# Performance work log

Measured on AMD Instinct MI355X. Metric: run time of the kernel, lower is better.

## Reference

```python
import jax, jax.numpy as jnp
import numpy as np

MASK_VALUE = -10000000.0


def setup_inputs() -> dict:
    key = jax.random.key(0)
    ks = jax.random.split(key, 8)
    U, I, J, C, E = 128, 256, 512, 128, 128
    return {
        "target_items_context": jax.random.normal(ks[0], (U, I, C), jnp.float32),
        "interacted_items_context": jax.random.normal(ks[1], (U, J, C), jnp.float32),
        "user_embeds": jax.random.normal(ks[2], (U, E), jnp.float32),
        "attention_mask": jax.random.randint(ks[3], (U, J), 0, 2) > 0,
        "w_dense": jax.random.normal(ks[4], (2 * C,), jnp.float32) * 0.02,
        "b_dense": jax.random.normal(ks[5], (1,), jnp.float32) * 0.02,
        "W_mlp": jax.random.normal(ks[6], (E + C, C), jnp.float32) * 0.02,
        "b_mlp": jax.random.normal(ks[7], (C,), jnp.float32) * 0.02,
    }


def reference(target_items_context, interacted_items_context, user_embeds,
              attention_mask, w_dense, b_dense, W_mlp, b_mlp):
    C = target_items_context.shape[-1]
    E = user_embeds.shape[-1]
    # additive attention score: tanh([t; k] @ w + b) = tanh(t@w1 + k@w2 + b)
    # (dropout is identity in eval mode)
    s_t = jnp.einsum('uic,c->ui', target_items_context, w_dense[:C])      # (U, I)
    s_k = jnp.einsum('ujc,c->uj', interacted_items_context, w_dense[C:])  # (U, J)
    scores = jnp.tanh(s_t[:, :, None] + s_k[:, None, :] + b_dense[0])     # (U, I, J)
    scores = scores + (~attention_mask)[:, None, :].astype(scores.dtype) * MASK_VALUE
    attn = jax.nn.softmax(scores, axis=-1)                                # (U, I, J)
    # weighted pooling of interacted contexts
    pooled = jnp.einsum('uij,ujc->uic', attn, interacted_items_context)   # (U, I, C)
    # mlp: relu([user; pooled] @ W + b) = relu(user@W[:E] + pooled@W[E:] + b)
    u_part = user_embeds @ W_mlp[:E]                                      # (U, C)
    user_context = jax.nn.relu(u_part[:, None, :] + pooled @ W_mlp[E:] + b_mlp)
    return user_context, attn
```

## Files before the change

kernel.cpp:

```cpp
#include <hip/hip_runtime.h>

#define UU 128
#define II 256
#define JJ 512
#define CC 128
#define EE 128
#define IB 16
#define NIB 16
#define JT 64
#define NJT 8
#define VTP 72

typedef short bf16x8 __attribute__((ext_vector_type(8)));
typedef float f32x4 __attribute__((ext_vector_type(4)));

union FragU { bf16x8 v; unsigned u[4]; };

__device__ __forceinline__ float fast_tanh(float x) {
    float ex = __expf(2.0f * x);
    return 1.0f - 2.0f / (ex + 1.0f);
}

__device__ __forceinline__ unsigned pack_bf16x2(float lo, float hi) {
    unsigned ul = __float_as_uint(lo), uh = __float_as_uint(hi);
    ul = (ul + 0x7FFFu + ((ul >> 16) & 1u)) >> 16;
    uh = (uh + 0x7FFFu + ((uh >> 16) & 1u)) >> 16;
    return ul | (uh << 16);
}

__device__ __forceinline__ short bf16s(float f) {
    unsigned u = __float_as_uint(f);
    u = (u + 0x7FFFu + ((u >> 16) & 1u)) >> 16;
    return (short)u;
}

__device__ __forceinline__ float wave_reduce_add(float v) {
#pragma unroll
    for (int k = 32; k >= 1; k >>= 1) v += __shfl_xor(v, k, 64);
    return v;
}

#define VT_BLOCKS (UU * NJT)
#define UP_BLOCKS (UU * CC / 256)

__global__ void precompute_kernel(const float* __restrict__ itc,
                                  const float* __restrict__ user,
                                  const float* __restrict__ wd,
                                  const float* __restrict__ Wm,
                                  const float* __restrict__ bm,
                                  float* __restrict__ sk_g,
                                  float* __restrict__ up_g,
                                  short* __restrict__ vtg,
                                  short* __restrict__ wtg) {
    __shared__ float vt_f[JT][CC + 4];
    int b = blockIdx.x;
    int t = threadIdx.x;
    if (b < VT_BLOCKS) {
        int u = b & 127, jt = b >> 7;
        const float* src = itc + ((size_t)u * JJ + jt * JT) * CC;
#pragma unroll
        for (int k = 0; k < 8; ++k) {
            int f = t + 256 * k;
            int row = f >> 5, c4 = (f & 31) * 4;
            f32x4 v = __builtin_nontemporal_load(
                (const f32x4*)&src[(size_t)row * CC + c4]);
            *(f32x4*)&vt_f[row][c4] = v;
        }
        __syncthreads();
        {
            int r = t >> 2, q4 = t & 3;
            float s = 0.f;
#pragma unroll
            for (int cc = 0; cc < 32; cc += 4) {
                float4 a = *(const float4*)&vt_f[r][q4 * 32 + cc];
                float4 w = *(const float4*)&wd[CC + q4 * 32 + cc];
                s += a.x * w.x + a.y * w.y + a.z * w.z + a.w * w.w;
            }
            s += __shfl_xor(s, 1, 64);
            s += __shfl_xor(s, 2, 64);
            if (q4 == 0) sk_g[u * JJ + jt * JT + r] = s;
        }
        {
            int c = t & 127, half = t >> 7;
            unsigned* dst = (unsigned*)(vtg + (size_t)(u * NJT + jt) * 8192) +
                            half * 2048 + c * 16;
#pragma unroll
            for (int m4 = 0; m4 < 4; ++m4) {
                unsigned q[4];
#pragma unroll
                for (int mm = 0; mm < 4; ++mm) {
                    int m = 4 * m4 + mm;
                    q[mm] = pack_bf16x2(vt_f[32 * half + 2 * m][c],
                                        vt_f[32 * half + 2 * m + 1][c]);
                }
                *(uint4*)&dst[4 * m4] = make_uint4(q[0], q[1], q[2], q[3]);
            }
        }
    } else if (b < VT_BLOCKS + UP_BLOCKS) {
        int idx = (b - VT_BLOCKS) * 256 + t;
        int u = idx >> 7, c = idx & 127;
        float acc = bm[c];
#pragma unroll 8
        for (int e = 0; e < EE; ++e) acc += user[u * EE + e] * Wm[e * CC + c];
        up_g[idx] = acc;
    } else {
        int n = t & 127, khalf = t >> 7;
#pragma unroll
        for (int ks2 = 0; ks2 < 2; ++ks2) {
            int ks = khalf * 2 + ks2;
#pragma unroll
            for (int g = 0; g < 4; ++g) {
                unsigned q[4];
#pragma unroll
                for (int pr = 0; pr < 4; ++pr) {
                    float lo = Wm[(size_t)(EE + 32 * ks + 8 * g + 2 * pr) * CC + n];
                    float hi = Wm[(size_t)(EE + 32 * ks + 8 * g + 2 * pr + 1) * CC + n];
                    q[pr] = pack_bf16x2(lo, hi);
                }
                *(uint4*)&wtg[ks * 4096 + n * 32 + 8 * g] =
                    make_uint4(q[0], q[1], q[2], q[3]);
            }
        }
    }
}

__global__ __launch_bounds__(256, 6) void fused_main(
    const float* __restrict__ tgt, const int* __restrict__ mask,
    const float* __restrict__ wd, const float* __restrict__ bd,
    const float* __restrict__ sk_g, const float* __restrict__ up_g,
    const short* __restrict__ vt_g, const short* __restrict__ wt_g,
    float* __restrict__ out_ctx, float* __restrict__ out_attn) {
    __shared__ __align__(16) short ps[8192];
    __shared__ __align__(16) short pooled_bf[2048];
    __shared__ float dinv_lds[IB];

    int b = blockIdx.x;
    int x = b & 7, qq = b >> 3;
    int u = x + 8 * (qq >> 4);
    int ib = qq & 15;
    int i0 = ib * IB;
    int t = threadIdx.x;
    int w = t >> 6, l = t & 63, ln = l & 15, g = l >> 4;
    int r = t >> 4, s4 = t & 15;

    float sv;
    {
        const float* trow = tgt + ((size_t)(u * II + i0 + r)) * CC + s4 * 8;
        f32x4 t0 = __builtin_nontemporal_load((const f32x4*)&trow[0]);
        f32x4 t1 = __builtin_nontemporal_load((const f32x4*)&trow[4]);
        float4 w0 = *(const float4*)&wd[s4 * 8];
        float4 w1 = *(const float4*)&wd[s4 * 8 + 4];
        float part = t0[0] * w0.x + t0[1] * w0.y + t0[2] * w0.z + t0[3] * w0.w +
                     t1[0] * w1.x + t1[1] * w1.y + t1[2] * w1.z + t1[3] * w1.w;
        part += __shfl_xor(part, 1, 64);
        part += __shfl_xor(part, 2, 64);
        part += __shfl_xor(part, 4, 64);
        part += __shfl_xor(part, 8, 64);
        sv = part + bd[0];
    }

    const float* skb = sk_g + u * JJ;
    const int* mkb = mask + u * JJ;
    float rowsum = 0.f;
#pragma unroll
    for (int h = 0; h < 4; ++h) {
        int jb = 8 * (s4 + 16 * h);
        float4 k0 = *(const float4*)&skb[jb];
        float4 k1 = *(const float4*)&skb[jb + 4];
        int4 m0 = *(const int4*)&mkb[jb];
        int4 m1 = *(const int4*)&mkb[jb + 4];
        float p0 = m0.x ? __expf(fast_tanh(sv + k0.x)) : 0.f;
        float p1 = m0.y ? __expf(fast_tanh(sv + k0.y)) : 0.f;
        float p2 = m0.z ? __expf(fast_tanh(sv + k0.z)) : 0.f;
        float p3 = m0.w ? __expf(fast_tanh(sv + k0.w)) : 0.f;
        float p4 = m1.x ? __expf(fast_tanh(sv + k1.x)) : 0.f;
        float p5 = m1.y ? __expf(fast_tanh(sv + k1.y)) : 0.f;
        float p6 = m1.z ? __expf(fast_tanh(sv + k1.z)) : 0.f;
        float p7 = m1.w ? __expf(fast_tanh(sv + k1.w)) : 0.f;
        rowsum += p0 + p1 + p2 + p3 + p4 + p5 + p6 + p7;
        unsigned q0 = pack_bf16x2(p0, p1);
        unsigned q1 = pack_bf16x2(p2, p3);
        unsigned q2 = pack_bf16x2(p4, p5);
        unsigned q3 = pack_bf16x2(p6, p7);
        int gp = (s4 + 16 * h) ^ (r & 7);
        *(uint4*)((char*)ps + r * 1024 + 16 * gp) = make_uint4(q0, q1, q2, q3);
    }
    rowsum += __shfl_xor(rowsum, 1, 64);
    rowsum += __shfl_xor(rowsum, 2, 64);
    rowsum += __shfl_xor(rowsum, 4, 64);
    rowsum += __shfl_xor(rowsum, 8, 64);
    float dinv = 1.0f / rowsum;
    if (s4 == 0) dinv_lds[r] = dinv;

    const short* b_base =
        vt_g + (size_t)u * (NJT * 8192) + (32 * w + ln) * 32 + 8 * g;
    bf16x8 pb0[4], pb1[4];
#pragma unroll
    for (int s = 0; s < 4; ++s) {
        int off = (s >> 1) * 8192 + (s & 1) * 4096;
        pb0[s] = *(const bf16x8*)&b_base[off];
        pb1[s] = *(const bf16x8*)&b_base[off + 512];
    }

    {
        float* ab = out_attn + ((size_t)(u * II + i0 + r)) * JJ;
#pragma unroll
        for (int h = 0; h < 4; ++h) {
            int gp = (s4 + 16 * h) ^ (r & 7);
            uint4 q = *(const uint4*)((char*)ps + r * 1024 + 16 * gp);
            int jb = 8 * (s4 + 16 * h);
            f32x4 v0, v1;
            v0[0] = __uint_as_float(q.x << 16) * dinv;
            v0[1] = __uint_as_float(q.x & 0xFFFF0000u) * dinv;
            v0[2] = __uint_as_float(q.y << 16) * dinv;
            v0[3] = __uint_as_float(q.y & 0xFFFF0000u) * dinv;
            v1[0] = __uint_as_float(q.z << 16) * dinv;
            v1[1] = __uint_as_float(q.z & 0xFFFF0000u) * dinv;
            v1[2] = __uint_as_float(q.w << 16) * dinv;
            v1[3] = __uint_as_float(q.w & 0xFFFF0000u) * dinv;
            __builtin_nontemporal_store(v0, (f32x4*)&ab[jb]);
            __builtin_nontemporal_store(v1, (f32x4*)&ab[jb + 4]);
        }
    }

    asm volatile("s_waitcnt lgkmcnt(0)" ::: "memory");
    __builtin_amdgcn_s_barrier();
    asm volatile("" ::: "memory");

    f32x4 acc0 = {0.f, 0.f, 0.f, 0.f};
    f32x4 acc1 = {0.f, 0.f, 0.f, 0.f};
    __builtin_amdgcn_s_setprio(1);
#pragma unroll
    for (int s = 0; s < 16; ++s) {
        bf16x8 af = *(const bf16x8*)((const char*)ps + ln * 1024 +
                                     16 * ((4 * s + g) ^ (ln & 7)));
        acc0 = __builtin_amdgcn_mfma_f32_16x16x32_bf16(af, pb0[s & 3], acc0, 0, 0, 0);
        acc1 = __builtin_amdgcn_mfma_f32_16x16x32_bf16(af, pb1[s & 3], acc1, 0, 0, 0);
        if (s < 12) {
            int off = ((s + 4) >> 1) * 8192 + ((s + 4) & 1) * 4096;
            pb0[s & 3] = *(const bf16x8*)&b_base[off];
            pb1[s & 3] = *(const bf16x8*)&b_base[off + 512];
        }
    }
    __builtin_amdgcn_s_setprio(0);

    const short* wbase = wt_g + (32 * w + ln) * 32 + 8 * g;
    bf16x8 wb0[4], wb1[4];
#pragma unroll
    for (int ks = 0; ks < 4; ++ks) {
        wb0[ks] = *(const bf16x8*)&wbase[ks * 4096];
        wb1[ks] = *(const bf16x8*)&wbase[ks * 4096 + 512];
    }

#pragma unroll
    for (int ri = 0; ri < 4; ++ri) {
        int row = 4 * g + ri;
        float dv = dinv_lds[row];
        int c0 = 32 * w + ln;
        int by0 = row * 256 + 16 * ((c0 >> 3) ^ (row & 7)) + 2 * (ln & 7);
        *(short*)((char*)pooled_bf + by0) = bf16s(acc0[ri] * dv);
        int c1 = c0 + 16;
        int by1 = row * 256 + 16 * ((c1 >> 3) ^ (row & 7)) + 2 * (ln & 7);
        *(short*)((char*)pooled_bf + by1) = bf16s(acc1[ri] * dv);
    }
    asm volatile("s_waitcnt lgkmcnt(0)" ::: "memory");
    __builtin_amdgcn_s_barrier();
    asm volatile("" ::: "memory");

    f32x4 oa0 = {0.f, 0.f, 0.f, 0.f};
    f32x4 oa1 = {0.f, 0.f, 0.f, 0.f};
#pragma unroll
    for (int ks = 0; ks < 4; ++ks) {
        bf16x8 pa = *(const bf16x8*)((const char*)pooled_bf + ln * 256 +
                                     16 * ((4 * ks + g) ^ (ln & 7)));
        oa0 = __builtin_amdgcn_mfma_f32_16x16x32_bf16(pa, wb0[ks], oa0, 0, 0, 0);
        oa1 = __builtin_amdgcn_mfma_f32_16x16x32_bf16(pa, wb1[ks], oa1, 0, 0, 0);
    }
    {
        int c0 = 32 * w + ln, c1 = c0 + 16;
        float up0v = up_g[u * CC + c0];
        float up1v = up_g[u * CC + c1];
        float* ctx = out_ctx + ((size_t)(u * II + i0)) * CC;
#pragma unroll
        for (int ri = 0; ri < 4; ++ri) {
            int row = 4 * g + ri;
            __builtin_nontemporal_store(fmaxf(oa0[ri] + up0v, 0.f),
                                        &ctx[(size_t)row * CC + c0]);
            __builtin_nontemporal_store(fmaxf(oa1[ri] + up1v, 0.f),
                                        &ctx[(size_t)row * CC + c1]);
        }
    }
}

__global__ __launch_bounds__(256, 3) void fused_fallback(
    const float* __restrict__ tgt, const float* __restrict__ itc,
    const float* __restrict__ user, const int* __restrict__ mask,
    const float* __restrict__ wd, const float* __restrict__ bd,
    const float* __restrict__ Wm, const float* __restrict__ bm,
    float* __restrict__ out_ctx, float* __restrict__ out_attn) {
    __shared__ __align__(16) short Vt[CC][VTP];
    __shared__ __align__(16) float pool[IB][CC + 4];
    __shared__ __align__(16) float skv[JJ];
    __shared__ __align__(16) float stv[IB];
    __shared__ __align__(16) float upv[CC];
    __shared__ __align__(16) float dinv_lds[IB];
    __shared__ unsigned char mk[JJ];

    int b = blockIdx.x;
    int x = b & 7, q = b >> 3;
    int u = x + 8 * (q >> 4);
    int ib = q & 15;
    int i0 = ib * IB;
    int t = threadIdx.x;

    mk[t] = (unsigned char)(mask[u * JJ + t] != 0);
    mk[t + 256] = (unsigned char)(mask[u * JJ + t + 256] != 0);

    {
        int lane = t & 63, w4 = t >> 6;
        float2 w2 = *(const float2*)&wd[CC + lane * 2];
        for (int r = w4; r < JJ; r += 4) {
            float2 a = *(const float2*)&itc[((size_t)u * JJ + r) * CC + lane * 2];
            float s = wave_reduce_add(a.x * w2.x + a.y * w2.y);
            if (lane == 0) skv[r] = s;
        }
        float2 w1 = *(const float2*)&wd[lane * 2];
        float bdv = bd[0];
        for (int r = w4; r < IB; r += 4) {
            float2 a = *(const float2*)&tgt[((size_t)u * II + i0 + r) * CC + lane * 2];
            float s = wave_reduce_add(a.x * w1.x + a.y * w1.y);
            if (lane == 0) stv[r] = s + bdv;
        }
        if (t < CC) {
            float acc = bm[t];
            for (int e = 0; e < EE; ++e) acc += user[u * EE + e] * Wm[e * CC + t];
            upv[t] = acc;
        }
    }
    __syncthreads();

    const int l = t & 63;
    const int w = t >> 6;
    const int ln = l & 15;
    const int g = l >> 4;

    bf16x8 a[16];
    float rowsum = 0.0f;
    {
        float s = stv[ln];
#pragma unroll
        for (int t16 = 0; t16 < 16; ++t16) {
            int j = 32 * t16 + 8 * g;
            float4 k0 = *(const float4*)&skv[j];
            float4 k1 = *(const float4*)&skv[j + 4];
            unsigned m0 = *(const unsigned*)&mk[j];
            unsigned m1 = *(const unsigned*)&mk[j + 4];
            float pf[8];
            pf[0] = (m0 & 0x000000FFu) ? __expf(fast_tanh(s + k0.x)) : 0.0f;
            pf[1] = (m0 & 0x0000FF00u) ? __expf(fast_tanh(s + k0.y)) : 0.0f;
            pf[2] = (m0 & 0x00FF0000u) ? __expf(fast_tanh(s + k0.z)) : 0.0f;
            pf[3] = (m0 & 0xFF000000u) ? __expf(fast_tanh(s + k0.w)) : 0.0f;
            pf[4] = (m1 & 0x000000FFu) ? __expf(fast_tanh(s + k1.x)) : 0.0f;
            pf[5] = (m1 & 0x0000FF00u) ? __expf(fast_tanh(s + k1.y)) : 0.0f;
            pf[6] = (m1 & 0x00FF0000u) ? __expf(fast_tanh(s + k1.z)) : 0.0f;
            pf[7] = (m1 & 0xFF000000u) ? __expf(fast_tanh(s + k1.w)) : 0.0f;
            rowsum += pf[0] + pf[1] + pf[2] + pf[3] + pf[4] + pf[5] + pf[6] + pf[7];
            FragU cu;
            cu.u[0] = pack_bf16x2(pf[0], pf[1]);
            cu.u[1] = pack_bf16x2(pf[2], pf[3]);
            cu.u[2] = pack_bf16x2(pf[4], pf[5]);
            cu.u[3] = pack_bf16x2(pf[6], pf[7]);
            a[t16] = cu.v;
        }
    }
    rowsum += __shfl_xor(rowsum, 16, 64);
    rowsum += __shfl_xor(rowsum, 32, 64);
    float dinv = 1.0f / rowsum;
    if (t < 16) dinv_lds[t] = dinv;

    {
        float* abase = out_attn + ((size_t)(u * II + i0 + ln)) * JJ + 8 * g;
#pragma unroll
        for (int t16 = 0; t16 < 16; ++t16) {
            FragU cu; cu.v = a[t16];
            float f0 = __uint_as_float(cu.u[0] << 16) * dinv;
            float f1 = __uint_as_float(cu.u[0] & 0xFFFF0000u) * dinv;
            float f2 = __uint_as_float(cu.u[1] << 16) * dinv;
            float f3 = __uint_as_float(cu.u[1] & 0xFFFF0000u) * dinv;
            float f4 = __uint_as_float(cu.u[2] << 16) * dinv;
            float f5 = __uint_as_float(cu.u[2] & 0xFFFF0000u) * dinv;
            float f6 = __uint_as_float(cu.u[3] << 16) * dinv;
            float f7 = __uint_as_float(cu.u[3] & 0xFFFF0000u) * dinv;
            *(float4*)&abase[32 * t16] = make_float4(f0, f1, f2, f3);
            *(float4*)&abase[32 * t16 + 4] = make_float4(f4, f5, f6, f7);
        }
    }

    f32x4 acc0 = {0.f, 0.f, 0.f, 0.f};
    f32x4 acc1 = {0.f, 0.f, 0.f, 0.f};
    const float* Vu = itc + (size_t)u * JJ * CC;
    const int cg = t & 31;
    const int jp = t >> 5;
    const int n0 = w * 32;

    for (int jt = 0; jt < 8; ++jt) {
        int j0 = jt * JT;
        __syncthreads();
#pragma unroll
        for (int it = 0; it < 4; ++it) {
            int jl = 2 * (jp + 8 * it);
            const float* r0 = &Vu[(size_t)(j0 + jl) * CC];
            const float* r1 = r0 + CC;
#pragma unroll
            for (int qv = 0; qv < 4; ++qv) {
                int c = cg + 32 * qv;
                *(unsigned*)&Vt[c][jl] = pack_bf16x2(r0[c], r1[c]);
            }
        }
        __syncthreads();
#pragma unroll
        for (int kk = 0; kk < 2; ++kk) {
            bf16x8 b0 = *(const bf16x8*)&Vt[n0 + ln][32 * kk + 8 * g];
            bf16x8 b1 = *(const bf16x8*)&Vt[n0 + 16 + ln][32 * kk + 8 * g];
            acc0 = __builtin_amdgcn_mfma_f32_16x16x32_bf16(a[2 * jt + kk], b0,
                                                           acc0, 0, 0, 0);
            acc1 = __builtin_amdgcn_mfma_f32_16x16x32_bf16(a[2 * jt + kk], b1,
                                                           acc1, 0, 0, 0);
        }
    }

    __syncthreads();
    {
        float4 dv = *(const float4*)&dinv_lds[4 * g];
        float dvr[4] = {dv.x, dv.y, dv.z, dv.w};
#pragma unroll
        for (int r = 0; r < 4; ++r) {
            pool[4 * g + r][n0 + ln] = acc0[r] * dvr[r];
            pool[4 * g + r][n0 + 16 + ln] = acc1[r] * dvr[r];
        }
    }
    __syncthreads();

    {
        int tx = t & 15, ty = t >> 4;
        float o[8];
#pragma unroll
        for (int k = 0; k < 8; ++k) o[k] = 0.f;
#pragma unroll 4
        for (int k = 0; k < CC; ++k) {
            float pk = pool[ty][k];
            float4 w0 = *(const float4*)&Wm[(size_t)(EE + k) * CC + tx * 8];
            float4 w1 = *(const float4*)&Wm[(size_t)(EE + k) * CC + tx * 8 + 4];
            o[0] += pk * w0.x; o[1] += pk * w0.y; o[2] += pk * w0.z; o[3] += pk * w0.w;
            o[4] += pk * w1.x; o[5] += pk * w1.y; o[6] += pk * w1.z; o[7] += pk * w1.w;
        }
        float4 up0 = *(const float4*)&upv[tx * 8];
        float4 up1 = *(const float4*)&upv[tx * 8 + 4];
        float4 r0, r1;
        r0.x = fmaxf(o[0] + up0.x, 0.f); r0.y = fmaxf(o[1] + up0.y, 0.f);
        r0.z = fmaxf(o[2] + up0.z, 0.f); r0.w = fmaxf(o[3] + up0.w, 0.f);
        r1.x = fmaxf(o[4] + up1.x, 0.f); r1.y = fmaxf(o[5] + up1.y, 0.f);
        r1.z = fmaxf(o[6] + up1.z, 0.f); r1.w = fmaxf(o[7] + up1.w, 0.f);
        float* ctx = out_ctx + ((size_t)(u * II + i0 + ty)) * CC + tx * 8;
        *(float4*)&ctx[0] = r0;
        *(float4*)&ctx[4] = r1;
    }
}

extern "C" void kernel_launch(void* const* d_in, const int* in_sizes, int n_in,
                              void* d_out, int out_size, void* d_ws,
                              size_t ws_size, hipStream_t stream) {
    const float* tgt  = (const float*)d_in[0];
    const float* itc  = (const float*)d_in[1];
    const float* user = (const float*)d_in[2];
    const int*   mask = (const int*)d_in[3];
    const float* wd   = (const float*)d_in[4];
    const float* bd   = (const float*)d_in[5];
    const float* Wm   = (const float*)d_in[6];
    const float* bm   = (const float*)d_in[7];
    float* out_ctx  = (float*)d_out;
    float* out_attn = out_ctx + (size_t)UU * II * CC;

    size_t scalars = (size_t)(UU * JJ + UU * CC) * sizeof(float);
    size_t vt_bytes = (size_t)UU * NJT * 8192 * sizeof(short);
    size_t wt_bytes = (size_t)16384 * sizeof(short);
    size_t need = scalars + vt_bytes + wt_bytes;
    if (ws_size >= need) {
        float* sk_g = (float*)d_ws;
        float* up_g = sk_g + UU * JJ;
        short* vt_g = (short*)((char*)d_ws + scalars);
        short* wt_g = vt_g + (size_t)UU * NJT * 8192;
        int gridA = VT_BLOCKS + UP_BLOCKS + 1;
        precompute_kernel<<<gridA, 256, 0, stream>>>(itc, user, wd, Wm, bm,
                                                     sk_g, up_g, vt_g, wt_g);
        fused_main<<<UU * NIB, 256, 0, stream>>>(tgt, mask, wd, bd, sk_g, up_g,
                                                 vt_g, wt_g, out_ctx, out_attn);
    } else {
        fused_fallback<<<UU * NIB, 256, 0, stream>>>(
            tgt, itc, user, mask, wd, bd, Wm, bm, out_ctx, out_attn);
    }
}
```

Measured before the change: 58.06 us.

## Process 32 target rows per block to reuse V fragments across two MFMA tiles

The main fused kernel now handles 32 target rows per block instead of 16, halving the grid and reusing each loaded V (interacted-context) B-fragment and MLP weight fragment for two 16-row MFMA tiles. The attention-probability write-out moves after the pooling MFMA loop, now reads from LDS per row with a flat thread mapping, and the pooled buffer aliases the probability LDS region through an extra barrier. This cuts global loads of V and W per output row in exchange for doubled LDS use (32KB), fewer resident blocks per CU, and more registers per thread.

```diff
diff --git a/kernel.cpp b/kernel.cpp
--- a/kernel.cpp
+++ b/kernel.cpp
@@ -5,11 +5,12 @@
 #define JJ 512
 #define CC 128
 #define EE 128
-#define IB 16
-#define NIB 16
+#define IB2 32
+#define NIB2 8
 #define JT 64
 #define NJT 8
 #define VTP 72
+#define IBF 16
 
 typedef short bf16x8 __attribute__((ext_vector_type(8)));
 typedef float f32x4 __attribute__((ext_vector_type(4)));
@@ -124,47 +125,54 @@
     }
 }
 
-__global__ __launch_bounds__(256, 6) void fused_main(
+__global__ __launch_bounds__(256, 4) void fused_main(
     const float* __restrict__ tgt, const int* __restrict__ mask,
     const float* __restrict__ wd, const float* __restrict__ bd,
     const float* __restrict__ sk_g, const float* __restrict__ up_g,
     const short* __restrict__ vt_g, const short* __restrict__ wt_g,
     float* __restrict__ out_ctx, float* __restrict__ out_attn) {
-    __shared__ __align__(16) short ps[8192];
-    __shared__ __align__(16) short pooled_bf[2048];
-    __shared__ float dinv_lds[IB];
+    __shared__ __align__(16) short ps[16384];
+    __shared__ float dinv_lds[IB2];
 
     int b = blockIdx.x;
-    int x = b & 7, qq = b >> 3;
-    int u = x + 8 * (qq >> 4);
-    int ib = qq & 15;
-    int i0 = ib * IB;
+    int x = b & 7, q = b >> 3;
+    int u = x + 8 * (q >> 3);
+    int ib = q & 7;
+    int i0 = ib * IB2;
     int t = threadIdx.x;
     int w = t >> 6, l = t & 63, ln = l & 15, g = l >> 4;
-    int r = t >> 4, s4 = t & 15;
+    int r2 = t >> 3, seg8 = t & 7;
+    int tile = r2 >> 4, rr = r2 & 15;
 
     float sv;
     {
-        const float* trow = tgt + ((size_t)(u * II + i0 + r)) * CC + s4 * 8;
+        const float* trow = tgt + ((size_t)(u * II + i0 + r2)) * CC + seg8 * 16;
         f32x4 t0 = __builtin_nontemporal_load((const f32x4*)&trow[0]);
         f32x4 t1 = __builtin_nontemporal_load((const f32x4*)&trow[4]);
-        float4 w0 = *(const float4*)&wd[s4 * 8];
-        float4 w1 = *(const float4*)&wd[s4 * 8 + 4];
+        f32x4 t2 = __builtin_nontemporal_load((const f32x4*)&trow[8]);
+        f32x4 t3 = __builtin_nontemporal_load((const f32x4*)&trow[12]);
+        float4 w0 = *(const float4*)&wd[seg8 * 16];
+        float4 w1 = *(const float4*)&wd[seg8 * 16 + 4];
+        float4 w2 = *(const float4*)&wd[seg8 * 16 + 8];
+        float4 w3 = *(const float4*)&wd[seg8 * 16 + 12];
         float part = t0[0] * w0.x + t0[1] * w0.y + t0[2] * w0.z + t0[3] * w0.w +
-                     t1[0] * w1.x + t1[1] * w1.y + t1[2] * w1.z + t1[3] * w1.w;
+                     t1[0] * w1.x + t1[1] * w1.y + t1[2] * w1.z + t1[3] * w1.w +
+                     t2[0] * w2.x + t2[1] * w2.y + t2[2] * w2.z + t2[3] * w2.w +
+                     t3[0] * w3.x + t3[1] * w3.y + t3[2] * w3.z + t3[3] * w3.w;
         part += __shfl_xor(part, 1, 64);
         part += __shfl_xor(part, 2, 64);
         part += __shfl_xor(part, 4, 64);
-        part += __shfl_xor(part, 8, 64);
         sv = part + bd[0];
     }
 
     const float* skb = sk_g + u * JJ;
     const int* mkb = mask + u * JJ;
+    char* psrow = (char*)ps + tile * 16384 + rr * 1024;
     float rowsum = 0.f;
-#pragma unroll
-    for (int h = 0; h < 4; ++h) {
-        int jb = 8 * (s4 + 16 * h);
+#pragma unroll 4
+    for (int h = 0; h < 8; ++h) {
+        int gcol = seg8 + 8 * h;
+        int jb = gcol * 8;
         float4 k0 = *(const float4*)&skb[jb];
         float4 k1 = *(const float4*)&skb[jb + 4];
         int4 m0 = *(const int4*)&mkb[jb];
@@ -182,15 +190,13 @@
         unsigned q1 = pack_bf16x2(p2, p3);
         unsigned q2 = pack_bf16x2(p4, p5);
         unsigned q3 = pack_bf16x2(p6, p7);
-        int gp = (s4 + 16 * h) ^ (r & 7);
-        *(uint4*)((char*)ps + r * 1024 + 16 * gp) = make_uint4(q0, q1, q2, q3);
+        int gp = gcol ^ (rr & 7);
+        *(uint4*)(psrow + 16 * gp) = make_uint4(q0, q1, q2, q3);
     }
     rowsum += __shfl_xor(rowsum, 1, 64);
     rowsum += __shfl_xor(rowsum, 2, 64);
     rowsum += __shfl_xor(rowsum, 4, 64);
-    rowsum += __shfl_xor(rowsum, 8, 64);
-    float dinv = 1.0f / rowsum;
-    if (s4 == 0) dinv_lds[r] = dinv;
+    if (seg8 == 0) dinv_lds[r2] = 1.0f / rowsum;
 
     const short* b_base =
         vt_g + (size_t)u * (NJT * 8192) + (32 * w + ln) * 32 + 8 * g;
@@ -202,40 +208,22 @@
         pb1[s] = *(const bf16x8*)&b_base[off + 512];
     }
 
-    {
-        float* ab = out_attn + ((size_t)(u * II + i0 + r)) * JJ;
-#pragma unroll
-        for (int h = 0; h < 4; ++h) {
-            int gp = (s4 + 16 * h) ^ (r & 7);
-            uint4 q = *(const uint4*)((char*)ps + r * 1024 + 16 * gp);
-            int jb = 8 * (s4 + 16 * h);
-            f32x4 v0, v1;
-            v0[0] = __uint_as_float(q.x << 16) * dinv;
-            v0[1] = __uint_as_float(q.x & 0xFFFF0000u) * dinv;
-            v0[2] = __uint_as_float(q.y << 16) * dinv;
-            v0[3] = __uint_as_float(q.y & 0xFFFF0000u) * dinv;
-            v1[0] = __uint_as_float(q.z << 16) * dinv;
-            v1[1] = __uint_as_float(q.z & 0xFFFF0000u) * dinv;
-            v1[2] = __uint_as_float(q.w << 16) * dinv;
-            v1[3] = __uint_as_float(q.w & 0xFFFF0000u) * dinv;
-            __builtin_nontemporal_store(v0, (f32x4*)&ab[jb]);
-            __builtin_nontemporal_store(v1, (f32x4*)&ab[jb + 4]);
-        }
-    }
-
     asm volatile("s_waitcnt lgkmcnt(0)" ::: "memory");
     __builtin_amdgcn_s_barrier();
     asm volatile("" ::: "memory");
 
-    f32x4 acc0 = {0.f, 0.f, 0.f, 0.f};
-    f32x4 acc1 = {0.f, 0.f, 0.f, 0.f};
+    f32x4 a00 = {0.f, 0.f, 0.f, 0.f}, a01 = {0.f, 0.f, 0.f, 0.f};
+    f32x4 a10 = {0.f, 0.f, 0.f, 0.f}, a11 = {0.f, 0.f, 0.f, 0.f};
     __builtin_amdgcn_s_setprio(1);
 #pragma unroll
     for (int s = 0; s < 16; ++s) {
-        bf16x8 af = *(const bf16x8*)((const char*)ps + ln * 1024 +
-                                     16 * ((4 * s + g) ^ (ln & 7)));
-        acc0 = __builtin_amdgcn_mfma_f32_16x16x32_bf16(af, pb0[s & 3], acc0, 0, 0, 0);
-        acc1 = __builtin_amdgcn_mfma_f32_16x16x32_bf16(af, pb1[s & 3], acc1, 0, 0, 0);
+        int abyte = ln * 1024 + 16 * ((4 * s + g) ^ (ln & 7));
+        bf16x8 af0 = *(const bf16x8*)((const char*)ps + abyte);
+        bf16x8 af1 = *(const bf16x8*)((const char*)ps + 16384 + abyte);
+        a00 = __builtin_amdgcn_mfma_f32_16x16x32_bf16(af0, pb0[s & 3], a00, 0, 0, 0);
+        a01 = __builtin_amdgcn_mfma_f32_16x16x32_bf16(af0, pb1[s & 3], a01, 0, 0, 0);
+        a10 = __builtin_amdgcn_mfma_f32_16x16x32_bf16(af1, pb0[s & 3], a10, 0, 0, 0);
+        a11 = __builtin_amdgcn_mfma_f32_16x16x32_bf16(af1, pb1[s & 3], a11, 0, 0, 0);
         if (s < 12) {
             int off = ((s + 4) >> 1) * 8192 + ((s + 4) & 1) * 4096;
             pb0[s & 3] = *(const bf16x8*)&b_base[off];
@@ -244,6 +232,27 @@
     }
     __builtin_amdgcn_s_setprio(0);
 
+    {
+        float* ab = out_attn + ((size_t)(u * II + i0)) * JJ;
+#pragma unroll
+        for (int k = 0; k < 16; ++k) {
+            int f = t + 256 * k;
+            int row = f >> 7;
+            int j4 = (f & 127) * 4;
+            int gcol = j4 >> 3, half = (j4 >> 2) & 1;
+            int tl = row >> 4, rw = row & 15;
+            uint2 qv = *(const uint2*)((const char*)ps + tl * 16384 + rw * 1024 +
+                                       16 * (gcol ^ (rw & 7)) + 8 * half);
+            float dv = dinv_lds[row];
+            f32x4 v;
+            v[0] = __uint_as_float(qv.x << 16) * dv;
+            v[1] = __uint_as_float(qv.x & 0xFFFF0000u) * dv;
+            v[2] = __uint_as_float(qv.y << 16) * dv;
+            v[3] = __uint_as_float(qv.y & 0xFFFF0000u) * dv;
+            __builtin_nontemporal_store(v, (f32x4*)&ab[(size_t)row * JJ + j4]);
+        }
+    }
+
     const short* wbase = wt_g + (32 * w + ln) * 32 + 8 * g;
     bf16x8 wb0[4], wb1[4];
 #pragma unroll
@@ -252,29 +261,42 @@
         wb1[ks] = *(const bf16x8*)&wbase[ks * 4096 + 512];
     }
 
-#pragma unroll
-    for (int ri = 0; ri < 4; ++ri) {
-        int row = 4 * g + ri;
-        float dv = dinv_lds[row];
-        int c0 = 32 * w + ln;
-        int by0 = row * 256 + 16 * ((c0 >> 3) ^ (row & 7)) + 2 * (ln & 7);
-        *(short*)((char*)pooled_bf + by0) = bf16s(acc0[ri] * dv);
-        int c1 = c0 + 16;
-        int by1 = row * 256 + 16 * ((c1 >> 3) ^ (row & 7)) + 2 * (ln & 7);
-        *(short*)((char*)pooled_bf + by1) = bf16s(acc1[ri] * dv);
-    }
     asm volatile("s_waitcnt lgkmcnt(0)" ::: "memory");
     __builtin_amdgcn_s_barrier();
     asm volatile("" ::: "memory");
 
-    f32x4 oa0 = {0.f, 0.f, 0.f, 0.f};
-    f32x4 oa1 = {0.f, 0.f, 0.f, 0.f};
+    {
+        char* pool = (char*)ps;
+        int c0 = 32 * w + ln, c1 = c0 + 16;
+#pragma unroll
+        for (int ri = 0; ri < 4; ++ri) {
+            int row0 = 4 * g + ri, row1 = 16 + row0;
+            float dv0 = dinv_lds[row0], dv1 = dinv_lds[row1];
+            *(short*)(pool + row0 * 256 + 16 * ((c0 >> 3) ^ (row0 & 7)) +
+                      2 * (ln & 7)) = bf16s(a00[ri] * dv0);
+            *(short*)(pool + row0 * 256 + 16 * ((c1 >> 3) ^ (row0 & 7)) +
+                      2 * (ln & 7)) = bf16s(a01[ri] * dv0);
+            *(short*)(pool + row1 * 256 + 16 * ((c0 >> 3) ^ (row1 & 7)) +
+                      2 * (ln & 7)) = bf16s(a10[ri] * dv1);
+            *(short*)(pool + row1 * 256 + 16 * ((c1 >> 3) ^ (row1 & 7)) +
+                      2 * (ln & 7)) = bf16s(a11[ri] * dv1);
+        }
+    }
+    asm volatile("s_waitcnt lgkmcnt(0)" ::: "memory");
+    __builtin_amdgcn_s_barrier();
+    asm volatile("" ::: "memory");
+
+    f32x4 o00 = {0.f, 0.f, 0.f, 0.f}, o01 = {0.f, 0.f, 0.f, 0.f};
+    f32x4 o10 = {0.f, 0.f, 0.f, 0.f}, o11 = {0.f, 0.f, 0.f, 0.f};
 #pragma unroll
     for (int ks = 0; ks < 4; ++ks) {
-        bf16x8 pa = *(const bf16x8*)((const char*)pooled_bf + ln * 256 +
-                                     16 * ((4 * ks + g) ^ (ln & 7)));
-        oa0 = __builtin_amdgcn_mfma_f32_16x16x32_bf16(pa, wb0[ks], oa0, 0, 0, 0);
-        oa1 = __builtin_amdgcn_mfma_f32_16x16x32_bf16(pa, wb1[ks], oa1, 0, 0, 0);
+        int pbyte0 = ln * 256 + 16 * ((4 * ks + g) ^ (ln & 7));
+        bf16x8 pa0 = *(const bf16x8*)((const char*)ps + pbyte0);
+        bf16x8 pa1 = *(const bf16x8*)((const char*)ps + 4096 + pbyte0);
+        o00 = __builtin_amdgcn_mfma_f32_16x16x32_bf16(pa0, wb0[ks], o00, 0, 0, 0);
+        o01 = __builtin_amdgcn_mfma_f32_16x16x32_bf16(pa0, wb1[ks], o01, 0, 0, 0);
+        o10 = __builtin_amdgcn_mfma_f32_16x16x32_bf16(pa1, wb0[ks], o10, 0, 0, 0);
+        o11 = __builtin_amdgcn_mfma_f32_16x16x32_bf16(pa1, wb1[ks], o11, 0, 0, 0);
     }
     {
         int c0 = 32 * w + ln, c1 = c0 + 16;
@@ -283,11 +305,15 @@
         float* ctx = out_ctx + ((size_t)(u * II + i0)) * CC;
 #pragma unroll
         for (int ri = 0; ri < 4; ++ri) {
-            int row = 4 * g + ri;
-            __builtin_nontemporal_store(fmaxf(oa0[ri] + up0v, 0.f),
-                                        &ctx[(size_t)row * CC + c0]);
-            __builtin_nontemporal_store(fmaxf(oa1[ri] + up1v, 0.f),
-                                        &ctx[(size_t)row * CC + c1]);
+            int row0 = 4 * g + ri, row1 = 16 + row0;
+            __builtin_nontemporal_store(fmaxf(o00[ri] + up0v, 0.f),
+                                        &ctx[(size_t)row0 * CC + c0]);
+            __builtin_nontemporal_store(fmaxf(o01[ri] + up1v, 0.f),
+                                        &ctx[(size_t)row0 * CC + c1]);
+            __builtin_nontemporal_store(fmaxf(o10[ri] + up0v, 0.f),
+                                        &ctx[(size_t)row1 * CC + c0]);
+            __builtin_nontemporal_store(fmaxf(o11[ri] + up1v, 0.f),
+                                        &ctx[(size_t)row1 * CC + c1]);
         }
     }
 }
@@ -299,18 +325,18 @@
     const float* __restrict__ Wm, const float* __restrict__ bm,
     float* __restrict__ out_ctx, float* __restrict__ out_attn) {
     __shared__ __align__(16) short Vt[CC][VTP];
-    __shared__ __align__(16) float pool[IB][CC + 4];
+    __shared__ __align__(16) float pool[IBF][CC + 4];
     __shared__ __align__(16) float skv[JJ];
-    __shared__ __align__(16) float stv[IB];
+    __shared__ __align__(16) float stv[IBF];
     __shared__ __align__(16) float upv[CC];
-    __shared__ __align__(16) float dinv_lds[IB];
+    __shared__ __align__(16) float dinv_lds[IBF];
     __shared__ unsigned char mk[JJ];
 
     int b = blockIdx.x;
     int x = b & 7, q = b >> 3;
     int u = x + 8 * (q >> 4);
     int ib = q & 15;
-    int i0 = ib * IB;
+    int i0 = ib * IBF;
     int t = threadIdx.x;
 
     mk[t] = (unsigned char)(mask[u * JJ + t] != 0);
@@ -326,7 +352,7 @@
         }
         float2 w1 = *(const float2*)&wd[lane * 2];
         float bdv = bd[0];
-        for (int r = w4; r < IB; r += 4) {
+        for (int r = w4; r < IBF; r += 4) {
             float2 a = *(const float2*)&tgt[((size_t)u * II + i0 + r) * CC + lane * 2];
             float s = wave_reduce_add(a.x * w1.x + a.y * w1.y);
             if (lane == 0) stv[r] = s + bdv;
@@ -493,10 +519,10 @@
         int gridA = VT_BLOCKS + UP_BLOCKS + 1;
         precompute_kernel<<<gridA, 256, 0, stream>>>(itc, user, wd, Wm, bm,
                                                      sk_g, up_g, vt_g, wt_g);
-        fused_main<<<UU * NIB, 256, 0, stream>>>(tgt, mask, wd, bd, sk_g, up_g,
-                                                 vt_g, wt_g, out_ctx, out_attn);
+        fused_main<<<UU * NIB2, 256, 0, stream>>>(tgt, mask, wd, bd, sk_g, up_g,
+                                                  vt_g, wt_g, out_ctx, out_attn);
     } else {
-        fused_fallback<<<UU * NIB, 256, 0, stream>>>(
+        fused_fallback<<<UU * (II / IBF), 256, 0, stream>>>(
             tgt, itc, user, mask, wd, bd, Wm, bm, out_ctx, out_attn);
     }
 }
```

Measured after the change: 49.50 us (median of 3 runs). 1.17x faster.

## Restructure main kernel into 512-thread blocks staging full V tile in LDS

Applied to the files above, without the earlier changes.

The main kernel now launches 256 blocks of 512 threads, each covering 128 target rows of one user, instead of 2048 blocks of 16 rows. The whole bf16 V tile for the user (128 KB) is staged once into LDS and reused by all eight waves, so the same V data is no longer re-read from global memory by 16 separate blocks. Softmax probabilities stay in registers as MFMA A-fragments rather than passing through LDS, and each wave computes all 128 output columns. In exchange, occupancy drops to one block per CU with heavy LDS and register use. The grid of 256 blocks is also only about the CU count, so latency hiding and load balance may suffer.

```diff
diff --git a/kernel.cpp b/kernel.cpp
--- a/kernel.cpp
+++ b/kernel.cpp
@@ -5,11 +5,10 @@
 #define JJ 512
 #define CC 128
 #define EE 128
-#define IB 16
-#define NIB 16
 #define JT 64
 #define NJT 8
 #define VTP 72
+#define IBF 16
 
 typedef short bf16x8 __attribute__((ext_vector_type(8)));
 typedef float f32x4 __attribute__((ext_vector_type(4)));
@@ -124,102 +123,100 @@
     }
 }
 
-__global__ __launch_bounds__(256, 6) void fused_main(
+__global__ __launch_bounds__(512, 1) void fused_main(
     const float* __restrict__ tgt, const int* __restrict__ mask,
     const float* __restrict__ wd, const float* __restrict__ bd,
     const float* __restrict__ sk_g, const float* __restrict__ up_g,
     const short* __restrict__ vt_g, const short* __restrict__ wt_g,
     float* __restrict__ out_ctx, float* __restrict__ out_attn) {
-    __shared__ __align__(16) short ps[8192];
-    __shared__ __align__(16) short pooled_bf[2048];
-    __shared__ float dinv_lds[IB];
+    __shared__ __align__(16) short Vt[65536];
 
     int b = blockIdx.x;
-    int x = b & 7, qq = b >> 3;
-    int u = x + 8 * (qq >> 4);
-    int ib = qq & 15;
-    int i0 = ib * IB;
+    int u = b & 127, half = b >> 7;
+    int i0 = half * 128;
     int t = threadIdx.x;
     int w = t >> 6, l = t & 63, ln = l & 15, g = l >> 4;
-    int r = t >> 4, s4 = t & 15;
+    int irow = i0 + w * 16 + ln;
+
+    const float* trow = tgt + ((size_t)(u * II + irow)) * CC + g * 32;
+    f32x4 tv[8];
+#pragma unroll
+    for (int k = 0; k < 8; ++k)
+        tv[k] = __builtin_nontemporal_load((const f32x4*)&trow[4 * k]);
+
+    const short* vsrc = vt_g + (size_t)u * 65536;
+    {
+        bf16x8 stg[16];
+#pragma unroll
+        for (int k = 0; k < 16; ++k)
+            stg[k] = *(const bf16x8*)&vsrc[t * 8 + 4096 * k];
+#pragma unroll
+        for (int k = 0; k < 16; ++k)
+            *(bf16x8*)&Vt[t * 8 + 4096 * k] = stg[k];
+    }
 
     float sv;
     {
-        const float* trow = tgt + ((size_t)(u * II + i0 + r)) * CC + s4 * 8;
-        f32x4 t0 = __builtin_nontemporal_load((const f32x4*)&trow[0]);
-        f32x4 t1 = __builtin_nontemporal_load((const f32x4*)&trow[4]);
-        float4 w0 = *(const float4*)&wd[s4 * 8];
-        float4 w1 = *(const float4*)&wd[s4 * 8 + 4];
-        float part = t0[0] * w0.x + t0[1] * w0.y + t0[2] * w0.z + t0[3] * w0.w +
-                     t1[0] * w1.x + t1[1] * w1.y + t1[2] * w1.z + t1[3] * w1.w;
-        part += __shfl_xor(part, 1, 64);
-        part += __shfl_xor(part, 2, 64);
-        part += __shfl_xor(part, 4, 64);
-        part += __shfl_xor(part, 8, 64);
+        float part = 0.f;
+#pragma unroll
+        for (int k = 0; k < 8; ++k) {
+            float4 wv = *(const float4*)&wd[g * 32 + 4 * k];
+            part += tv[k][0] * wv.x + tv[k][1] * wv.y + tv[k][2] * wv.z +
+                    tv[k][3] * wv.w;
+        }
+        part += __shfl_xor(part, 16, 64);
+        part += __shfl_xor(part, 32, 64);
         sv = part + bd[0];
     }
 
     const float* skb = sk_g + u * JJ;
     const int* mkb = mask + u * JJ;
+    bf16x8 a[16];
     float rowsum = 0.f;
 #pragma unroll
-    for (int h = 0; h < 4; ++h) {
-        int jb = 8 * (s4 + 16 * h);
-        float4 k0 = *(const float4*)&skb[jb];
-        float4 k1 = *(const float4*)&skb[jb + 4];
-        int4 m0 = *(const int4*)&mkb[jb];
-        int4 m1 = *(const int4*)&mkb[jb + 4];
-        float p0 = m0.x ? __expf(fast_tanh(sv + k0.x)) : 0.f;
-        float p1 = m0.y ? __expf(fast_tanh(sv + k0.y)) : 0.f;
-        float p2 = m0.z ? __expf(fast_tanh(sv + k0.z)) : 0.f;
-        float p3 = m0.w ? __expf(fast_tanh(sv + k0.w)) : 0.f;
-        float p4 = m1.x ? __expf(fast_tanh(sv + k1.x)) : 0.f;
-        float p5 = m1.y ? __expf(fast_tanh(sv + k1.y)) : 0.f;
-        float p6 = m1.z ? __expf(fast_tanh(sv + k1.z)) : 0.f;
-        float p7 = m1.w ? __expf(fast_tanh(sv + k1.w)) : 0.f;
-        rowsum += p0 + p1 + p2 + p3 + p4 + p5 + p6 + p7;
-        unsigned q0 = pack_bf16x2(p0, p1);
-        unsigned q1 = pack_bf16x2(p2, p3);
-        unsigned q2 = pack_bf16x2(p4, p5);
-        unsigned q3 = pack_bf16x2(p6, p7);
-        int gp = (s4 + 16 * h) ^ (r & 7);
-        *(uint4*)((char*)ps + r * 1024 + 16 * gp) = make_uint4(q0, q1, q2, q3);
-    }
-    rowsum += __shfl_xor(rowsum, 1, 64);
-    rowsum += __shfl_xor(rowsum, 2, 64);
-    rowsum += __shfl_xor(rowsum, 4, 64);
-    rowsum += __shfl_xor(rowsum, 8, 64);
+    for (int t16 = 0; t16 < 16; ++t16) {
+        int j = 32 * t16 + 8 * g;
+        float4 k0 = *(const float4*)&skb[j];
+        float4 k1 = *(const float4*)&skb[j + 4];
+        int4 m0 = *(const int4*)&mkb[j];
+        int4 m1 = *(const int4*)&mkb[j + 4];
+        float pf[8];
+        pf[0] = m0.x ? __expf(fast_tanh(sv + k0.x)) : 0.f;
+        pf[1] = m0.y ? __expf(fast_tanh(sv + k0.y)) : 0.f;
+        pf[2] = m0.z ? __expf(fast_tanh(sv + k0.z)) : 0.f;
+        pf[3] = m0.w ? __expf(fast_tanh(sv + k0.w)) : 0.f;
+        pf[4] = m1.x ? __expf(fast_tanh(sv + k1.x)) : 0.f;
+        pf[5] = m1.y ? __expf(fast_tanh(sv + k1.y)) : 0.f;
+        pf[6] = m1.z ? __expf(fast_tanh(sv + k1.z)) : 0.f;
+        pf[7] = m1.w ? __expf(fast_tanh(sv + k1.w)) : 0.f;
+        rowsum += pf[0] + pf[1] + pf[2] + pf[3] + pf[4] + pf[5] + pf[6] + pf[7];
+        FragU cu;
+        cu.u[0] = pack_bf16x2(pf[0], pf[1]);
+        cu.u[1] = pack_bf16x2(pf[2], pf[3]);
+        cu.u[2] = pack_bf16x2(pf[4], pf[5]);
+        cu.u[3] = pack_bf16x2(pf[6], pf[7]);
+        a[t16] = cu.v;
+    }
+    rowsum += __shfl_xor(rowsum, 16, 64);
+    rowsum += __shfl_xor(rowsum, 32, 64);
     float dinv = 1.0f / rowsum;
-    if (s4 == 0) dinv_lds[r] = dinv;
-
-    const short* b_base =
-        vt_g + (size_t)u * (NJT * 8192) + (32 * w + ln) * 32 + 8 * g;
-    bf16x8 pb0[4], pb1[4];
-#pragma unroll
-    for (int s = 0; s < 4; ++s) {
-        int off = (s >> 1) * 8192 + (s & 1) * 4096;
-        pb0[s] = *(const bf16x8*)&b_base[off];
-        pb1[s] = *(const bf16x8*)&b_base[off + 512];
-    }
-
-    {
-        float* ab = out_attn + ((size_t)(u * II + i0 + r)) * JJ;
-#pragma unroll
-        for (int h = 0; h < 4; ++h) {
-            int gp = (s4 + 16 * h) ^ (r & 7);
-            uint4 q = *(const uint4*)((char*)ps + r * 1024 + 16 * gp);
-            int jb = 8 * (s4 + 16 * h);
+
+    {
+        float* ab = out_attn + ((size_t)(u * II + irow)) * JJ + 8 * g;
+#pragma unroll
+        for (int t16 = 0; t16 < 16; ++t16) {
+            FragU cu; cu.v = a[t16];
             f32x4 v0, v1;
-            v0[0] = __uint_as_float(q.x << 16) * dinv;
-            v0[1] = __uint_as_float(q.x & 0xFFFF0000u) * dinv;
-            v0[2] = __uint_as_float(q.y << 16) * dinv;
-            v0[3] = __uint_as_float(q.y & 0xFFFF0000u) * dinv;
-            v1[0] = __uint_as_float(q.z << 16) * dinv;
-            v1[1] = __uint_as_float(q.z & 0xFFFF0000u) * dinv;
-            v1[2] = __uint_as_float(q.w << 16) * dinv;
-            v1[3] = __uint_as_float(q.w & 0xFFFF0000u) * dinv;
-            __builtin_nontemporal_store(v0, (f32x4*)&ab[jb]);
-            __builtin_nontemporal_store(v1, (f32x4*)&ab[jb + 4]);
+            v0[0] = __uint_as_float(cu.u[0] << 16) * dinv;
+            v0[1] = __uint_as_float(cu.u[0] & 0xFFFF0000u) * dinv;
+            v0[2] = __uint_as_float(cu.u[1] << 16) * dinv;
+            v0[3] = __uint_as_float(cu.u[1] & 0xFFFF0000u) * dinv;
+            v1[0] = __uint_as_float(cu.u[2] << 16) * dinv;
+            v1[1] = __uint_as_float(cu.u[2] & 0xFFFF0000u) * dinv;
+            v1[2] = __uint_as_float(cu.u[3] << 16) * dinv;
+            v1[3] = __uint_as_float(cu.u[3] & 0xFFFF0000u) * dinv;
+            __builtin_nontemporal_store(v0, (f32x4*)&ab[32 * t16]);
+            __builtin_nontemporal_store(v1, (f32x4*)&ab[32 * t16 + 4]);
         }
     }
 
@@ -227,67 +224,82 @@
     __builtin_amdgcn_s_barrier();
     asm volatile("" ::: "memory");
 
-    f32x4 acc0 = {0.f, 0.f, 0.f, 0.f};
-    f32x4 acc1 = {0.f, 0.f, 0.f, 0.f};
-    __builtin_amdgcn_s_setprio(1);
+    f32x4 acc[8];
+    {
+        f32x4 z = {0.f, 0.f, 0.f, 0.f};
+#pragma unroll
+        for (int n = 0; n < 8; ++n) acc[n] = z;
+    }
 #pragma unroll
     for (int s = 0; s < 16; ++s) {
-        bf16x8 af = *(const bf16x8*)((const char*)ps + ln * 1024 +
-                                     16 * ((4 * s + g) ^ (ln & 7)));
-        acc0 = __builtin_amdgcn_mfma_f32_16x16x32_bf16(af, pb0[s & 3], acc0, 0, 0, 0);
-        acc1 = __builtin_amdgcn_mfma_f32_16x16x32_bf16(af, pb1[s & 3], acc1, 0, 0, 0);
-        if (s < 12) {
-            int off = ((s + 4) >> 1) * 8192 + ((s + 4) & 1) * 4096;
-            pb0[s & 3] = *(const bf16x8*)&b_base[off];
-            pb1[s & 3] = *(const bf16x8*)&b_base[off + 512];
-        }
-    }
-    __builtin_amdgcn_s_setprio(0);
-
-    const short* wbase = wt_g + (32 * w + ln) * 32 + 8 * g;
-    bf16x8 wb0[4], wb1[4];
-#pragma unroll
-    for (int ks = 0; ks < 4; ++ks) {
-        wb0[ks] = *(const bf16x8*)&wbase[ks * 4096];
-        wb1[ks] = *(const bf16x8*)&wbase[ks * 4096 + 512];
-    }
-
-#pragma unroll
-    for (int ri = 0; ri < 4; ++ri) {
-        int row = 4 * g + ri;
-        float dv = dinv_lds[row];
-        int c0 = 32 * w + ln;
-        int by0 = row * 256 + 16 * ((c0 >> 3) ^ (row & 7)) + 2 * (ln & 7);
-        *(short*)((char*)pooled_bf + by0) = bf16s(acc0[ri] * dv);
-        int c1 = c0 + 16;
-        int by1 = row * 256 + 16 * ((c1 >> 3) ^ (row & 7)) + 2 * (ln & 7);
-        *(short*)((char*)pooled_bf + by1) = bf16s(acc1[ri] * dv);
-    }
+        int base = (s >> 1) * 16384 + (s & 1) * 8192 + 16 * g;
+#pragma unroll
+        for (int n = 0; n < 8; ++n) {
+            bf16x8 bf =
+                *(const bf16x8*)((const char*)Vt + base + (16 * n + ln) * 64);
+            acc[n] = __builtin_amdgcn_mfma_f32_16x16x32_bf16(a[s], bf, acc[n],
+                                                             0, 0, 0);
+        }
+    }
+
     asm volatile("s_waitcnt lgkmcnt(0)" ::: "memory");
     __builtin_amdgcn_s_barrier();
     asm volatile("" ::: "memory");
 
-    f32x4 oa0 = {0.f, 0.f, 0.f, 0.f};
-    f32x4 oa1 = {0.f, 0.f, 0.f, 0.f};
-#pragma unroll
-    for (int ks = 0; ks < 4; ++ks) {
-        bf16x8 pa = *(const bf16x8*)((const char*)pooled_bf + ln * 256 +
-                                     16 * ((4 * ks + g) ^ (ln & 7)));
-        oa0 = __builtin_amdgcn_mfma_f32_16x16x32_bf16(pa, wb0[ks], oa0, 0, 0, 0);
-        oa1 = __builtin_amdgcn_mfma_f32_16x16x32_bf16(pa, wb1[ks], oa1, 0, 0, 0);
-    }
-    {
-        int c0 = 32 * w + ln, c1 = c0 + 16;
-        float up0v = up_g[u * CC + c0];
-        float up1v = up_g[u * CC + c1];
-        float* ctx = out_ctx + ((size_t)(u * II + i0)) * CC;
-#pragma unroll
-        for (int ri = 0; ri < 4; ++ri) {
-            int row = 4 * g + ri;
-            __builtin_nontemporal_store(fmaxf(oa0[ri] + up0v, 0.f),
-                                        &ctx[(size_t)row * CC + c0]);
-            __builtin_nontemporal_store(fmaxf(oa1[ri] + up1v, 0.f),
-                                        &ctx[(size_t)row * CC + c1]);
+    char* pw = (char*)Vt + w * 4096;
+    {
+        float dvr[4];
+#pragma unroll
+        for (int ri = 0; ri < 4; ++ri) dvr[ri] = __shfl(dinv, 4 * g + ri, 64);
+#pragma unroll
+        for (int n = 0; n < 8; ++n) {
+            int c = 16 * n + ln;
+#pragma unroll
+            for (int ri = 0; ri < 4; ++ri) {
+                int row16 = 4 * g + ri;
+                *(short*)(pw + row16 * 256 + 16 * ((c >> 3) ^ (row16 & 7)) +
+                          2 * (c & 7)) = bf16s(acc[n][ri] * dvr[ri]);
+            }
+        }
+    }
+
+    f32x4 o[8];
+    {
+        f32x4 z = {0.f, 0.f, 0.f, 0.f};
+#pragma unroll
+        for (int n = 0; n < 8; ++n) o[n] = z;
+    }
+    bf16x8 pa[4];
+#pragma unroll
+    for (int ks = 0; ks < 4; ++ks)
+        pa[ks] = *(const bf16x8*)(pw + ln * 256 + 16 * ((4 * ks + g) & 15 ^ 0) +
+                                  0) ;
+#pragma unroll
+    for (int ks = 0; ks < 4; ++ks)
+        pa[ks] = *(const bf16x8*)(pw + ln * 256 +
+                                  16 * ((4 * ks + g) ^ (ln & 7)));
+#pragma unroll
+    for (int n = 0; n < 8; ++n) {
+#pragma unroll
+        for (int ks = 0; ks < 4; ++ks) {
+            bf16x8 wf =
+                *(const bf16x8*)&wt_g[ks * 4096 + (16 * n + ln) * 32 + 8 * g];
+            o[n] = __builtin_amdgcn_mfma_f32_16x16x32_bf16(pa[ks], wf, o[n],
+                                                           0, 0, 0);
+        }
+    }
+    {
+        float* ctx = out_ctx + ((size_t)(u * II + i0 + w * 16)) * CC;
+#pragma unroll
+        for (int n = 0; n < 8; ++n) {
+            float up = up_g[u * CC + 16 * n + ln];
+#pragma unroll
+            for (int ri = 0; ri < 4; ++ri) {
+                int row16 = 4 * g + ri;
+                __builtin_nontemporal_store(
+                    fmaxf(o[n][ri] + up, 0.f),
+                    &ctx[(size_t)row16 * CC + 16 * n + ln]);
+            }
         }
     }
 }
@@ -299,18 +311,18 @@
     const float* __restrict__ Wm, const float* __restrict__ bm,
     float* __restrict__ out_ctx, float* __restrict__ out_attn) {
     __shared__ __align__(16) short Vt[CC][VTP];
-    __shared__ __align__(16) float pool[IB][CC + 4];
+    __shared__ __align__(16) float pool[IBF][CC + 4];
     __shared__ __align__(16) float skv[JJ];
-    __shared__ __align__(16) float stv[IB];
+    __shared__ __align__(16) float stv[IBF];
     __shared__ __align__(16) float upv[CC];
-    __shared__ __align__(16) float dinv_lds[IB];
+    __shared__ __align__(16) float dinv_lds[IBF];
     __shared__ unsigned char mk[JJ];
 
     int b = blockIdx.x;
     int x = b & 7, q = b >> 3;
     int u = x + 8 * (q >> 4);
     int ib = q & 15;
-    int i0 = ib * IB;
+    int i0 = ib * IBF;
     int t = threadIdx.x;
 
     mk[t] = (unsigned char)(mask[u * JJ + t] != 0);
@@ -326,7 +338,7 @@
         }
         float2 w1 = *(const float2*)&wd[lane * 2];
         float bdv = bd[0];
-        for (int r = w4; r < IB; r += 4) {
+        for (int r = w4; r < IBF; r += 4) {
             float2 a = *(const float2*)&tgt[((size_t)u * II + i0 + r) * CC + lane * 2];
             float s = wave_reduce_add(a.x * w1.x + a.y * w1.y);
             if (lane == 0) stv[r] = s + bdv;
@@ -493,10 +505,10 @@
         int gridA = VT_BLOCKS + UP_BLOCKS + 1;
         precompute_kernel<<<gridA, 256, 0, stream>>>(itc, user, wd, Wm, bm,
                                                      sk_g, up_g, vt_g, wt_g);
-        fused_main<<<UU * NIB, 256, 0, stream>>>(tgt, mask, wd, bd, sk_g, up_g,
-                                                 vt_g, wt_g, out_ctx, out_attn);
+        fused_main<<<256, 512, 0, stream>>>(tgt, mask, wd, bd, sk_g, up_g,
+                                            vt_g, wt_g, out_ctx, out_attn);
     } else {
-        fused_fallback<<<UU * NIB, 256, 0, stream>>>(
+        fused_fallback<<<UU * (II / IBF), 256, 0, stream>>>(
             tgt, itc, user, mask, wd, bd, Wm, bm, out_ctx, out_attn);
     }
 }
```

After: 65.87 us. +13.4%, slower.
